# Kernel tuning notes

Hardware: AMD Instinct MI355X
Metric: run time of the kernel (lower is better)

The kernel has to match this reference:

```python
import jax, jax.numpy as jnp
import numpy as np

N_NODES = 50000
N_EDGES = 600000
D = 128
N_ETYPES = 8

def setup_inputs() -> dict:
    key = jax.random.key(0)
    ks = jax.random.split(key, 9)
    nfeat = jax.random.normal(ks[0], (N_NODES, D), dtype=jnp.float32)
    head_w = jax.random.normal(ks[1], (D,), dtype=jnp.float32) * 0.1
    head_b = jax.random.normal(ks[2], (1,), dtype=jnp.float32)
    tail_w = jax.random.normal(ks[3], (D,), dtype=jnp.float32) * 0.1
    tail_b = jax.random.normal(ks[4], (1,), dtype=jnp.float32)
    rel_w = jax.random.normal(ks[5], (N_ETYPES,), dtype=jnp.float32)
    src = jax.random.randint(ks[6], (N_EDGES,), 0, N_NODES, dtype=jnp.int32)
    dst = jax.random.randint(ks[7], (N_EDGES,), 0, N_NODES, dtype=jnp.int32)
    etype = jax.random.randint(ks[8], (N_EDGES,), 0, N_ETYPES, dtype=jnp.int32)
    return {"nfeat": nfeat, "head_w": head_w, "head_b": head_b,
            "tail_w": tail_w, "tail_b": tail_b, "rel_w": rel_w,
            "src": src, "dst": dst, "etype": etype}

def reference(nfeat, head_w, head_b, tail_w, tail_b, rel_w, src, dst, etype):
    n = nfeat.shape[0]
    # per-node scalar scores (el from head_weight, er from tail_weight)
    el = nfeat @ head_w + head_b[0]            # [N]
    er = nfeat @ tail_w + tail_b[0]            # [N]
    # per-edge logit: u_add_v plus relation bias
    logits = el[src] + er[dst] + rel_w[etype]  # [E]
    # edge_softmax grouped by destination node (stable)
    seg_max = jax.ops.segment_max(logits, dst, num_segments=n)
    ex = jnp.exp(logits - seg_max[dst])
    seg_sum = jax.ops.segment_sum(ex, dst, num_segments=n)
    a = ex / seg_sum[dst]                      # [E]
    # u_mul_e + scatter-sum aggregation
    out = jax.ops.segment_sum(a[:, None] * nfeat[src], dst, num_segments=n)  # [N, D]
    return out
```

## Files before the change

kernel.cpp:

```cpp
#include <hip/hip_runtime.h>

#define D 128
#define CSTRIDE 16

typedef float f32x4 __attribute__((ext_vector_type(4)));

#define Q8_SCALE   (7.0f / 127.0f)
#define Q8_INVS    (127.0f / 7.0f)

__device__ __forceinline__ int q8i(float v) {
    return __float2int_rn(fminf(fmaxf(v * Q8_INVS, -127.f), 127.f));
}

__global__ void scores_el(const float* __restrict__ nfeat,
                          const float* __restrict__ head_w,
                          const float* __restrict__ head_b,
                          float* __restrict__ el,
                          int4* __restrict__ cnt4,
                          int n4, int n_nodes) {
    int t = (int)(blockIdx.x * blockDim.x + threadIdx.x);

    for (int i = t; i < n4; i += (int)(gridDim.x * blockDim.x))
        cnt4[i] = make_int4(0, 0, 0, 0);

    int wave = t >> 6;
    int lane = threadIdx.x & 63;
    int half = lane >> 5;
    int fl   = lane & 31;
    int node = wave * 2 + half;
    if (node >= n_nodes) return;

    const float4 v  = ((const float4*)(nfeat + (size_t)node * D))[fl];
    const float4 hw = ((const float4*)head_w)[fl];

    float se = v.x * hw.x + v.y * hw.y + v.z * hw.z + v.w * hw.w;
    #pragma unroll
    for (int o = 16; o > 0; o >>= 1) se += __shfl_xor(se, o);
    if (fl == 0) el[node] = se + head_b[0];
}

__global__ void scatter_conv(const int* __restrict__ src,
                             const int* __restrict__ dst,
                             const int* __restrict__ etype,
                             const float* __restrict__ el,
                             const float* __restrict__ rel_w,
                             const float* __restrict__ nfeat,
                             unsigned* __restrict__ q8,
                             int* __restrict__ cnt,
                             int2* __restrict__ sorted,
                             int n_edges, int cap, int Sw, int T,
                             int n_nodes) {
    int g    = (int)((blockIdx.x * blockDim.x + threadIdx.x) >> 6);
    int lane = threadIdx.x & 63;
    if (g >= T) return;

    long long a = (long long)g * Sw;
    int fg  = (int)(a / T);
    int fg1 = (int)((a + Sw) / T);

    if (fg1 > fg) {
        int e = fg * 64 + lane;
        if (e < n_edges) {
            int s = src[e];
            int d = dst[e];
            float x = __expf(el[s] + rel_w[etype[e]]);
            int r = atomicAdd(&cnt[(size_t)d * CSTRIDE], 1);
            if (r < cap)
                sorted[(size_t)d * cap + r] = make_int2(s, __float_as_int(x));
        }
    } else {
        int j    = g - fg;
        int half = lane >> 5;
        int fl   = lane & 31;
        int node = j * 2 + half;
        if (node < n_nodes) {
            const float4 v = ((const float4*)(nfeat + (size_t)node * D))[fl];
            int a0 = q8i(v.x), a1 = q8i(v.y), a2 = q8i(v.z), a3 = q8i(v.w);
            unsigned pk = (unsigned)(a0 & 0xff)
                        | ((unsigned)(a1 & 0xff) << 8)
                        | ((unsigned)(a2 & 0xff) << 16)
                        | ((unsigned)(a3 & 0xff) << 24);
            q8[(size_t)node * 32 + fl] = pk;
        }
    }
}

__global__ void aggregate_q8(const uint2* __restrict__ q8,
                             const int* __restrict__ cnt,
                             const int2* __restrict__ sorted,
                             float* __restrict__ out,
                             int n_nodes, int cap) {
    int t64  = (int)(blockIdx.x * blockDim.x + threadIdx.x);
    int wave = t64 >> 6;
    int lane = threadIdx.x & 63;
    int q    = lane >> 4;
    int fl   = lane & 15;
    int node = wave * 4 + q;
    if (node >= n_nodes) return;

    int deg = cnt[(size_t)node * CSTRIDE];
    if (deg > cap) deg = cap;
    size_t b = (size_t)node * cap;

    float acc[8];
    #pragma unroll
    for (int i = 0; i < 8; ++i) acc[i] = 0.f;
    float ssum = 0.f;

    for (int k = 0; k < deg; k += 4) {
        int dm1 = deg - 1;
        int k1 = (k + 1 < deg) ? k + 1 : dm1;
        int k2 = (k + 2 < deg) ? k + 2 : dm1;
        int k3 = (k + 3 < deg) ? k + 3 : dm1;

        int2 p0 = sorted[b + k];
        int2 p1 = sorted[b + k1];
        int2 p2 = sorted[b + k2];
        int2 p3 = sorted[b + k3];

        float w0 = __int_as_float(p0.y);
        float w1 = (k + 1 < deg) ? __int_as_float(p1.y) : 0.f;
        float w2 = (k + 2 < deg) ? __int_as_float(p2.y) : 0.f;
        float w3 = (k + 3 < deg) ? __int_as_float(p3.y) : 0.f;

        const uint2 r0 = q8[(size_t)p0.x * 16 + fl];
        const uint2 r1 = q8[(size_t)p1.x * 16 + fl];
        const uint2 r2 = q8[(size_t)p2.x * 16 + fl];
        const uint2 r3 = q8[(size_t)p3.x * 16 + fl];

        #pragma unroll
        for (int j = 0; j < 4; ++j) {
            unsigned lo, hi; float wt;
            if      (j == 0) { lo = r0.x; hi = r0.y; wt = w0; }
            else if (j == 1) { lo = r1.x; hi = r1.y; wt = w1; }
            else if (j == 2) { lo = r2.x; hi = r2.y; wt = w2; }
            else             { lo = r3.x; hi = r3.y; wt = w3; }
            acc[0] += wt * (float)((int)(lo << 24) >> 24);
            acc[1] += wt * (float)((int)(lo << 16) >> 24);
            acc[2] += wt * (float)((int)(lo <<  8) >> 24);
            acc[3] += wt * (float)((int) lo        >> 24);
            acc[4] += wt * (float)((int)(hi << 24) >> 24);
            acc[5] += wt * (float)((int)(hi << 16) >> 24);
            acc[6] += wt * (float)((int)(hi <<  8) >> 24);
            acc[7] += wt * (float)((int) hi        >> 24);
        }
        ssum += (w0 + w1) + (w2 + w3);
    }

    float kf = (deg > 0) ? (Q8_SCALE / ssum) : 0.f;
    float* o = out + (size_t)node * D + fl * 8;
    f32x4 o0 = { acc[0]*kf, acc[1]*kf, acc[2]*kf, acc[3]*kf };
    f32x4 o1 = { acc[4]*kf, acc[5]*kf, acc[6]*kf, acc[7]*kf };
    __builtin_nontemporal_store(o0, (f32x4*)o);
    __builtin_nontemporal_store(o1, (f32x4*)(o + 4));
}


__global__ void hist_rank(const int* __restrict__ dst,
                          int* __restrict__ cnt,
                          int* __restrict__ rank,
                          int n_edges) {
    int t = (int)(blockIdx.x * blockDim.x + threadIdx.x);
    if (t < n_edges) {
        rank[t] = atomicAdd(&cnt[dst[t]], 1);
    }
}

__global__ void scan_offsets(const int* __restrict__ cnt,
                             int* __restrict__ off,
                             int n) {
    __shared__ int wsum[16];
    __shared__ int s_carry;
    int tid  = threadIdx.x;
    int lane = tid & 63;
    int wid  = tid >> 6;
    if (tid == 0) s_carry = 0;
    __syncthreads();

    for (int base = 0; base < n; base += 8192) {
        int i0 = base + tid * 8;
        int x[8];
        if (i0 + 7 < n) {
            int4 a = *(const int4*)(cnt + i0);
            int4 b = *(const int4*)(cnt + i0 + 4);
            x[0]=a.x; x[1]=a.y; x[2]=a.z; x[3]=a.w;
            x[4]=b.x; x[5]=b.y; x[6]=b.z; x[7]=b.w;
        } else {
            #pragma unroll
            for (int j = 0; j < 8; ++j) x[j] = (i0 + j < n) ? cnt[i0 + j] : 0;
        }
        int tsum = 0;
        #pragma unroll
        for (int j = 0; j < 8; ++j) tsum += x[j];

        int v = tsum;
        #pragma unroll
        for (int o = 1; o < 64; o <<= 1) {
            int y = __shfl_up(v, o);
            if (lane >= o) v += y;
        }
        if (lane == 63) wsum[wid] = v;
        __syncthreads();

        if (wid == 0 && lane < 16) {
            int w = wsum[lane];
            #pragma unroll
            for (int o = 1; o < 16; o <<= 1) {
                int y = __shfl_up(w, o);
                if (lane >= o) w += y;
            }
            wsum[lane] = w;
        }
        __syncthreads();

        int wave_excl = (wid == 0) ? 0 : wsum[wid - 1];
        int excl = s_carry + wave_excl + (v - tsum);

        if (i0 + 7 < n) {
            int4 o0, o1;
            int a = excl;
            o0.x = a; a += x[0];
            o0.y = a; a += x[1];
            o0.z = a; a += x[2];
            o0.w = a; a += x[3];
            o1.x = a; a += x[4];
            o1.y = a; a += x[5];
            o1.z = a; a += x[6];
            o1.w = a;
            *(int4*)(off + i0)     = o0;
            *(int4*)(off + i0 + 4) = o1;
        } else {
            int a = excl;
            #pragma unroll
            for (int j = 0; j < 8; ++j) {
                if (i0 + j < n) { off[i0 + j] = a; a += x[j]; }
            }
        }
        __syncthreads();
        if (tid == 0) s_carry += wsum[15];
        __syncthreads();
    }
    if (tid == 0) off[n] = s_carry;
}

__global__ void edge_sort(const int* __restrict__ src,
                          const int* __restrict__ dst,
                          const int* __restrict__ etype,
                          const int* __restrict__ rank,
                          const float* __restrict__ el,
                          const float* __restrict__ rel_w,
                          const int* __restrict__ off,
                          int2* __restrict__ sorted,
                          int n_edges) {
    int e = (int)(blockIdx.x * blockDim.x + threadIdx.x);
    if (e >= n_edges) return;
    int s = src[e];
    int d = dst[e];
    float x = __expf(el[s] + rel_w[etype[e]]);
    int p = off[d] + rank[e];
    sorted[p] = make_int2(s, __float_as_int(x));
}

__global__ void aggregate_f32(const float* __restrict__ nfeat,
                              const int* __restrict__ off,
                              const int2* __restrict__ sorted,
                              float* __restrict__ out,
                              int n_nodes) {
    int node = (int)((blockIdx.x * blockDim.x + threadIdx.x) >> 6);
    int lane = threadIdx.x & 63;
    if (node >= n_nodes) return;

    int b = off[node];
    int e = off[node + 1];

    float2 acc = make_float2(0.f, 0.f);
    float ssum = 0.f;
    int k = b;
    for (; k + 1 < e; k += 2) {
        int2 p0 = sorted[k];
        int2 p1 = sorted[k + 1];
        float w0 = __int_as_float(p0.y);
        float w1 = __int_as_float(p1.y);
        float2 v0 = ((const float2*)(nfeat + (size_t)p0.x * D))[lane];
        float2 v1 = ((const float2*)(nfeat + (size_t)p1.x * D))[lane];
        acc.x += w0 * v0.x + w1 * v1.x;
        acc.y += w0 * v0.y + w1 * v1.y;
        ssum  += w0 + w1;
    }
    if (k < e) {
        int2 p0 = sorted[k];
        float w0 = __int_as_float(p0.y);
        float2 v0 = ((const float2*)(nfeat + (size_t)p0.x * D))[lane];
        acc.x += w0 * v0.x;
        acc.y += w0 * v0.y;
        ssum  += w0;
    }
    float inv = (e > b) ? (1.0f / ssum) : 0.f;
    ((float2*)(out + (size_t)node * D))[lane] =
        make_float2(acc.x * inv, acc.y * inv);
}

extern "C" void kernel_launch(void* const* d_in, const int* in_sizes, int n_in,
                              void* d_out, int out_size, void* d_ws, size_t ws_size,
                              hipStream_t stream) {
    const float* nfeat  = (const float*)d_in[0];
    const float* head_w = (const float*)d_in[1];
    const float* head_b = (const float*)d_in[2];
    const float* rel_w  = (const float*)d_in[5];
    const int*   src    = (const int*)d_in[6];
    const int*   dst    = (const int*)d_in[7];
    const int*   etype  = (const int*)d_in[8];
    float* out = (float*)d_out;

    const int n_nodes = in_sizes[0] / D;
    const int n_edges = in_sizes[6];
    const int n_pad4  = (n_nodes + 3) & ~3;

    size_t fixed_bytes = (size_t)n_nodes * 4
                       + (size_t)n_pad4 * CSTRIDE * 4
                       + (size_t)n_nodes * 128;
    int cap = 0;
    for (int c : {64, 48, 40}) {
        if (ws_size >= fixed_bytes + (size_t)c * n_nodes * sizeof(int2)) {
            cap = c;
            break;
        }
    }

    if (cap > 0) {
        float*    el     = (float*)d_ws;
        int*      cnt    = (int*)(el + n_nodes);
        int2*     sorted = (int2*)(cnt + (size_t)n_pad4 * CSTRIDE);
        unsigned* q8     = (unsigned*)(sorted + (size_t)cap * n_nodes);

        {
            int n4 = n_pad4 * CSTRIDE / 4;
            long long threads = (long long)((n_nodes + 1) / 2) * 64;
            if (threads < n4) threads = n4;
            int blocks = (int)((threads + 255) / 256);
            scores_el<<<blocks, 256, 0, stream>>>(nfeat, head_w, head_b, el,
                                                  (int4*)cnt, n4, n_nodes);
        }
        {
            int Sw = (n_edges + 63) / 64;
            int Cw = (n_nodes + 1) / 2;
            int T  = Sw + Cw;
            int blocks = (T + 3) / 4;
            scatter_conv<<<blocks, 256, 0, stream>>>(src, dst, etype, el, rel_w,
                                                     nfeat, q8, cnt, sorted,
                                                     n_edges, cap, Sw, T, n_nodes);
        }
        {
            long long waves = (n_nodes + 3) / 4;
            int blocks = (int)((waves * 64 + 255) / 256);
            aggregate_q8<<<blocks, 256, 0, stream>>>((const uint2*)q8, cnt,
                                                     sorted, out, n_nodes, cap);
        }
        return;
    }

    float* el     = (float*)d_ws;
    int*   cnt    = (int*)(el + n_nodes);
    int*   off    = cnt + n_pad4;
    int*   rank   = off + n_nodes + 4;
    int2*  sorted = (int2*)(rank + n_edges);

    {
        int n4 = n_pad4 / 4;
        long long threads = (long long)((n_nodes + 1) / 2) * 64;
        if (threads < n4) threads = n4;
        int blocks = (int)((threads + 255) / 256);
        scores_el<<<blocks, 256, 0, stream>>>(nfeat, head_w, head_b, el,
                                              (int4*)cnt, n4, n_nodes);
    }
    {
        int blocks = (n_edges + 255) / 256;
        hist_rank<<<blocks, 256, 0, stream>>>(dst, cnt, rank, n_edges);
    }
    scan_offsets<<<1, 1024, 0, stream>>>(cnt, off, n_nodes);
    {
        int blocks = (n_edges + 255) / 256;
        edge_sort<<<blocks, 256, 0, stream>>>(src, dst, etype, rank,
                                              el, rel_w, off, sorted, n_edges);
    }
    {
        long long threads = (long long)n_nodes * 64;
        int blocks = (int)((threads + 255) / 256);
        aggregate_f32<<<blocks, 256, 0, stream>>>(nfeat, off, sorted, out, n_nodes);
    }
}
```

Measured before the change: 63.90 us.

## Defer edge weight exp to aggregation and pack src/etype into 32-bit buckets

The fast path no longer computes the edge weight in the scatter pass. It stores src<<3|etype as one 32-bit word per bucket slot, and the aggregation kernel recomputes exp(el[src]+rel_w[etype]). Because scatter no longer needs el, the el dot-product is fused into the quantization branch of the scatter kernel, leaving only a small zero-count kernel in front of it. The per-node counter padding (CSTRIDE 16) is removed, so counters are dense. The intent is to halve bucket traffic and remove a full pass over nfeat, at the cost of extra gathers and exp calls in aggregation and more atomic contention on the dense counters.

```diff
diff --git a/kernel.cpp b/kernel.cpp
--- a/kernel.cpp
+++ b/kernel.cpp
@@ -1,7 +1,6 @@
 #include <hip/hip_runtime.h>
 
 #define D 128
-#define CSTRIDE 16
 
 typedef float f32x4 __attribute__((ext_vector_type(4)));
 
@@ -12,44 +11,23 @@
     return __float2int_rn(fminf(fmaxf(v * Q8_INVS, -127.f), 127.f));
 }
 
-__global__ void scores_el(const float* __restrict__ nfeat,
-                          const float* __restrict__ head_w,
-                          const float* __restrict__ head_b,
-                          float* __restrict__ el,
-                          int4* __restrict__ cnt4,
-                          int n4, int n_nodes) {
-    int t = (int)(blockIdx.x * blockDim.x + threadIdx.x);
-
-    for (int i = t; i < n4; i += (int)(gridDim.x * blockDim.x))
-        cnt4[i] = make_int4(0, 0, 0, 0);
-
-    int wave = t >> 6;
-    int lane = threadIdx.x & 63;
-    int half = lane >> 5;
-    int fl   = lane & 31;
-    int node = wave * 2 + half;
-    if (node >= n_nodes) return;
-
-    const float4 v  = ((const float4*)(nfeat + (size_t)node * D))[fl];
-    const float4 hw = ((const float4*)head_w)[fl];
-
-    float se = v.x * hw.x + v.y * hw.y + v.z * hw.z + v.w * hw.w;
-    #pragma unroll
-    for (int o = 16; o > 0; o >>= 1) se += __shfl_xor(se, o);
-    if (fl == 0) el[node] = se + head_b[0];
-}
-
-__global__ void scatter_conv(const int* __restrict__ src,
-                             const int* __restrict__ dst,
-                             const int* __restrict__ etype,
-                             const float* __restrict__ el,
-                             const float* __restrict__ rel_w,
-                             const float* __restrict__ nfeat,
-                             unsigned* __restrict__ q8,
-                             int* __restrict__ cnt,
-                             int2* __restrict__ sorted,
-                             int n_edges, int cap, int Sw, int T,
-                             int n_nodes) {
+__global__ void zero_cnt(int4* __restrict__ cnt4, int n4) {
+    int i = (int)(blockIdx.x * blockDim.x + threadIdx.x);
+    if (i < n4) cnt4[i] = make_int4(0, 0, 0, 0);
+}
+
+__global__ void scatter_scores_conv(const int* __restrict__ src,
+                                    const int* __restrict__ dst,
+                                    const int* __restrict__ etype,
+                                    const float* __restrict__ nfeat,
+                                    const float* __restrict__ head_w,
+                                    const float* __restrict__ head_b,
+                                    float* __restrict__ el,
+                                    unsigned* __restrict__ q8,
+                                    int* __restrict__ cnt,
+                                    unsigned* __restrict__ bucket,
+                                    int n_edges, int cap, int Sw, int T,
+                                    int n_nodes) {
     int g    = (int)((blockIdx.x * blockDim.x + threadIdx.x) >> 6);
     int lane = threadIdx.x & 63;
     if (g >= T) return;
@@ -63,10 +41,10 @@
         if (e < n_edges) {
             int s = src[e];
             int d = dst[e];
-            float x = __expf(el[s] + rel_w[etype[e]]);
-            int r = atomicAdd(&cnt[(size_t)d * CSTRIDE], 1);
+            int t = etype[e];
+            int r = atomicAdd(&cnt[d], 1);
             if (r < cap)
-                sorted[(size_t)d * cap + r] = make_int2(s, __float_as_int(x));
+                bucket[(size_t)d * cap + r] = ((unsigned)s << 3) | (unsigned)t;
         }
     } else {
         int j    = g - fg;
@@ -74,20 +52,29 @@
         int fl   = lane & 31;
         int node = j * 2 + half;
         if (node < n_nodes) {
-            const float4 v = ((const float4*)(nfeat + (size_t)node * D))[fl];
+            const float4 v  = ((const float4*)(nfeat + (size_t)node * D))[fl];
+            const float4 hw = ((const float4*)head_w)[fl];
+
             int a0 = q8i(v.x), a1 = q8i(v.y), a2 = q8i(v.z), a3 = q8i(v.w);
             unsigned pk = (unsigned)(a0 & 0xff)
                         | ((unsigned)(a1 & 0xff) << 8)
                         | ((unsigned)(a2 & 0xff) << 16)
                         | ((unsigned)(a3 & 0xff) << 24);
             q8[(size_t)node * 32 + fl] = pk;
+
+            float se = v.x * hw.x + v.y * hw.y + v.z * hw.z + v.w * hw.w;
+            #pragma unroll
+            for (int o = 16; o > 0; o >>= 1) se += __shfl_xor(se, o);
+            if (fl == 0) el[node] = se + head_b[0];
         }
     }
 }
 
 __global__ void aggregate_q8(const uint2* __restrict__ q8,
                              const int* __restrict__ cnt,
-                             const int2* __restrict__ sorted,
+                             const unsigned* __restrict__ bucket,
+                             const float* __restrict__ el,
+                             const float* __restrict__ rel_w,
                              float* __restrict__ out,
                              int n_nodes, int cap) {
     int t64  = (int)(blockIdx.x * blockDim.x + threadIdx.x);
@@ -98,7 +85,7 @@
     int node = wave * 4 + q;
     if (node >= n_nodes) return;
 
-    int deg = cnt[(size_t)node * CSTRIDE];
+    int deg = cnt[node];
     if (deg > cap) deg = cap;
     size_t b = (size_t)node * cap;
 
@@ -113,20 +100,25 @@
         int k2 = (k + 2 < deg) ? k + 2 : dm1;
         int k3 = (k + 3 < deg) ? k + 3 : dm1;
 
-        int2 p0 = sorted[b + k];
-        int2 p1 = sorted[b + k1];
-        int2 p2 = sorted[b + k2];
-        int2 p3 = sorted[b + k3];
-
-        float w0 = __int_as_float(p0.y);
-        float w1 = (k + 1 < deg) ? __int_as_float(p1.y) : 0.f;
-        float w2 = (k + 2 < deg) ? __int_as_float(p2.y) : 0.f;
-        float w3 = (k + 3 < deg) ? __int_as_float(p3.y) : 0.f;
-
-        const uint2 r0 = q8[(size_t)p0.x * 16 + fl];
-        const uint2 r1 = q8[(size_t)p1.x * 16 + fl];
-        const uint2 r2 = q8[(size_t)p2.x * 16 + fl];
-        const uint2 r3 = q8[(size_t)p3.x * 16 + fl];
+        unsigned u0 = bucket[b + k];
+        unsigned u1 = bucket[b + k1];
+        unsigned u2 = bucket[b + k2];
+        unsigned u3 = bucket[b + k3];
+
+        int s0 = (int)(u0 >> 3), s1 = (int)(u1 >> 3);
+        int s2 = (int)(u2 >> 3), s3 = (int)(u3 >> 3);
+
+        const uint2 r0 = q8[(size_t)s0 * 16 + fl];
+        const uint2 r1 = q8[(size_t)s1 * 16 + fl];
+        const uint2 r2 = q8[(size_t)s2 * 16 + fl];
+        const uint2 r3 = q8[(size_t)s3 * 16 + fl];
+
+        float e0 = el[s0], e1 = el[s1], e2 = el[s2], e3 = el[s3];
+
+        float w0 = __expf(e0 + rel_w[u0 & 7u]);
+        float w1 = (k + 1 < deg) ? __expf(e1 + rel_w[u1 & 7u]) : 0.f;
+        float w2 = (k + 2 < deg) ? __expf(e2 + rel_w[u2 & 7u]) : 0.f;
+        float w3 = (k + 3 < deg) ? __expf(e3 + rel_w[u3 & 7u]) : 0.f;
 
         #pragma unroll
         for (int j = 0; j < 4; ++j) {
@@ -155,6 +147,31 @@
     __builtin_nontemporal_store(o1, (f32x4*)(o + 4));
 }
 
+
+__global__ void scores_el(const float* __restrict__ nfeat,
+                          const float* __restrict__ head_w,
+                          const float* __restrict__ head_b,
+                          float* __restrict__ el,
+                          int4* __restrict__ cnt4,
+                          int n4, int n_nodes) {
+    int t = (int)(blockIdx.x * blockDim.x + threadIdx.x);
+    for (int i = t; i < n4; i += (int)(gridDim.x * blockDim.x))
+        cnt4[i] = make_int4(0, 0, 0, 0);
+
+    int wave = t >> 6;
+    int lane = threadIdx.x & 63;
+    int half = lane >> 5;
+    int fl   = lane & 31;
+    int node = wave * 2 + half;
+    if (node >= n_nodes) return;
+
+    const float4 v  = ((const float4*)(nfeat + (size_t)node * D))[fl];
+    const float4 hw = ((const float4*)head_w)[fl];
+    float se = v.x * hw.x + v.y * hw.y + v.z * hw.z + v.w * hw.w;
+    #pragma unroll
+    for (int o = 16; o > 0; o >>= 1) se += __shfl_xor(se, o);
+    if (fl == 0) el[node] = se + head_b[0];
+}
 
 __global__ void hist_rank(const int* __restrict__ dst,
                           int* __restrict__ cnt,
@@ -312,51 +329,51 @@
     const int*   etype  = (const int*)d_in[8];
     float* out = (float*)d_out;
 
-    const int n_nodes = in_sizes[0] / D;
-    const int n_edges = in_sizes[6];
-    const int n_pad4  = (n_nodes + 3) & ~3;
-
-    size_t fixed_bytes = (size_t)n_nodes * 4
-                       + (size_t)n_pad4 * CSTRIDE * 4
-                       + (size_t)n_nodes * 128;
-    int cap = 0;
-    for (int c : {64, 48, 40}) {
-        if (ws_size >= fixed_bytes + (size_t)c * n_nodes * sizeof(int2)) {
-            cap = c;
-            break;
-        }
-    }
-
-    if (cap > 0) {
-        float*    el     = (float*)d_ws;
-        int*      cnt    = (int*)(el + n_nodes);
-        int2*     sorted = (int2*)(cnt + (size_t)n_pad4 * CSTRIDE);
-        unsigned* q8     = (unsigned*)(sorted + (size_t)cap * n_nodes);
-
-        {
-            int n4 = n_pad4 * CSTRIDE / 4;
-            long long threads = (long long)((n_nodes + 1) / 2) * 64;
-            if (threads < n4) threads = n4;
-            int blocks = (int)((threads + 255) / 256);
-            scores_el<<<blocks, 256, 0, stream>>>(nfeat, head_w, head_b, el,
-                                                  (int4*)cnt, n4, n_nodes);
-        }
-        {
-            int Sw = (n_edges + 63) / 64;
-            int Cw = (n_nodes + 1) / 2;
-            int T  = Sw + Cw;
-            int blocks = (T + 3) / 4;
-            scatter_conv<<<blocks, 256, 0, stream>>>(src, dst, etype, el, rel_w,
-                                                     nfeat, q8, cnt, sorted,
-                                                     n_edges, cap, Sw, T, n_nodes);
-        }
-        {
-            long long waves = (n_nodes + 3) / 4;
-            int blocks = (int)((waves * 64 + 255) / 256);
-            aggregate_q8<<<blocks, 256, 0, stream>>>((const uint2*)q8, cnt,
-                                                     sorted, out, n_nodes, cap);
-        }
-        return;
+    const int n_nodes  = in_sizes[0] / D;
+    const int n_edges  = in_sizes[6];
+    const int n_etypes = in_sizes[5];
+    const int n_pad4   = (n_nodes + 3) & ~3;
+
+    const bool can_pack = (n_etypes <= 8) && (n_nodes < (1 << 29));
+
+    if (can_pack) {
+        size_t fixed_bytes = (size_t)(n_nodes + n_pad4) * 4
+                           + (size_t)n_nodes * 128;
+        int cap = 0;
+        for (int c : {64, 48, 40}) {
+            if (ws_size >= fixed_bytes + (size_t)c * n_nodes * sizeof(unsigned)) {
+                cap = c;
+                break;
+            }
+        }
+        if (cap > 0) {
+            float*    el     = (float*)d_ws;
+            int*      cnt    = (int*)(el + n_nodes);
+            unsigned* bucket = (unsigned*)(cnt + n_pad4);
+            unsigned* q8     = bucket + (size_t)cap * n_nodes;
+
+            {
+                int n4 = n_pad4 / 4;
+                zero_cnt<<<(n4 + 255) / 256, 256, 0, stream>>>((int4*)cnt, n4);
+            }
+            {
+                int Sw = (n_edges + 63) / 64;
+                int Nw = (n_nodes + 1) / 2;
+                int T  = Sw + Nw;
+                int blocks = (T + 3) / 4;
+                scatter_scores_conv<<<blocks, 256, 0, stream>>>(
+                    src, dst, etype, nfeat, head_w, head_b,
+                    el, q8, cnt, bucket, n_edges, cap, Sw, T, n_nodes);
+            }
+            {
+                long long waves = (n_nodes + 3) / 4;
+                int blocks = (int)((waves * 64 + 255) / 256);
+                aggregate_q8<<<blocks, 256, 0, stream>>>((const uint2*)q8, cnt,
+                                                         bucket, el, rel_w,
+                                                         out, n_nodes, cap);
+            }
+            return;
+        }
     }
 
     float* el     = (float*)d_ws;
```

New measurement: 66.96 us. +4.8%, slower.
